# Optimization experiments

Hardware: AMD Instinct MI355X
Metric: run time of the kernel (lower is better)

## Reference

```python
import jax, jax.numpy as jnp
import numpy as np

HID = 16   # hidden_dim
K = 16     # kNN neighbors
B = 64     # graphs per batch
N_TS = 8192
N_LC = 12288


def setup_inputs() -> dict:
    key = jax.random.key(0)
    ks = jax.random.split(key, 24)

    def lin(k, fan_in, fan_out):
        w = jax.random.normal(k, (fan_in, fan_out), jnp.float32) / np.sqrt(fan_in).astype(np.float32)
        return w

    inp = {
        "x_ts": jax.random.normal(ks[0], (N_TS, 6), jnp.float32),
        "x_lc": jax.random.normal(ks[1], (N_LC, 5), jnp.float32),
        # balanced sorted graph ids -> every graph has >= K source nodes
        "batch_ts": jnp.repeat(jnp.arange(B, dtype=jnp.int32), N_TS // B),
        "batch_lc": jnp.repeat(jnp.arange(B, dtype=jnp.int32), N_LC // B),
        # ts_encode: Linear(6,16), ELU, Linear(16,16), ELU
        "ts_w1": lin(ks[2], 6, HID),  "ts_b1": jnp.zeros((HID,), jnp.float32),
        "ts_w2": lin(ks[3], HID, HID), "ts_b2": jnp.zeros((HID,), jnp.float32),
        # lc_encode: Linear(5,16), ELU, Linear(16,16), ELU
        "lc_w1": lin(ks[4], 5, HID),  "lc_b1": jnp.zeros((HID,), jnp.float32),
        "lc_w2": lin(ks[5], HID, HID), "lc_b2": jnp.zeros((HID,), jnp.float32),
        # EdgeConv nn: Linear(2*16, 16), ELU  (shared across the 3 conv calls)
        "conv_w": lin(ks[6], 2 * HID, HID), "conv_b": jnp.zeros((HID,), jnp.float32),
        # output MLP 16->64->32->8->4->1 (ELU between, none after last)
        "out_w1": lin(ks[7], HID, 64), "out_b1": jnp.zeros((64,), jnp.float32),
        "out_w2": lin(ks[8], 64, 32),  "out_b2": jnp.zeros((32,), jnp.float32),
        "out_w3": lin(ks[9], 32, 8),   "out_b3": jnp.zeros((8,), jnp.float32),
        "out_w4": lin(ks[10], 8, 4),   "out_b4": jnp.zeros((4,), jnp.float32),
        "out_w5": lin(ks[11], 4, 1),   "out_b5": jnp.zeros((1,), jnp.float32),
    }
    return inp


def _mlp2(x, w1, b1, w2, b2):
    return jax.nn.elu(jax.nn.elu(x @ w1 + b1) @ w2 + b2)


def _edge_conv(x_src, x_dst, b_src, b_dst, w, b):
    """DynamicEdgeConv: per-graph kNN of dst queries into src, message
    nn(cat[x_i, x_j - x_i]), max-aggregate over the K neighbors."""
    # squared distances [N_dst, N_src]
    d2 = (jnp.sum(x_dst * x_dst, 1)[:, None]
          - 2.0 * (x_dst @ x_src.T)
          + jnp.sum(x_src * x_src, 1)[None, :])
    d2 = jnp.where(b_dst[:, None] == b_src[None, :], d2, jnp.inf)
    _, idx = jax.lax.top_k(-d2, K)          # [N_dst, K] nearest (incl. self when src==dst)
    xj = x_src[idx]                          # [N_dst, K, H] gather
    xi = x_dst[:, None, :]                   # [N_dst, 1, H]
    msg = jnp.concatenate([jnp.broadcast_to(xi, xj.shape), xj - xi], axis=-1)
    msg = jax.nn.elu(msg @ w + b)            # [N_dst, K, H]
    return jnp.max(msg, axis=1)              # max aggregation -> [N_dst, H]


def reference(x_ts, x_lc, batch_ts, batch_lc,
              ts_w1, ts_b1, ts_w2, ts_b2,
              lc_w1, lc_b1, lc_w2, lc_b2,
              conv_w, conv_b,
              out_w1, out_b1, out_w2, out_b2, out_w3, out_b3,
              out_w4, out_b4, out_w5, out_b5):
    x_ts_enc = _mlp2(x_ts, ts_w1, ts_b1, ts_w2, ts_b2)   # [N_ts, 16]
    x_lc_enc = _mlp2(x_lc, lc_w1, lc_b1, lc_w2, lc_b2)   # [N_lc, 16]

    feats1 = _edge_conv(x_lc_enc, x_lc_enc, batch_lc, batch_lc, conv_w, conv_b)  # [N_lc,16]
    feats2 = _edge_conv(x_lc_enc, x_ts_enc, batch_lc, batch_ts, conv_w, conv_b)  # [N_ts,16]
    feats3 = _edge_conv(feats1,   feats2,   batch_lc, batch_ts, conv_w, conv_b)  # [N_ts,16]

    # avg_pool_x(batch_ts, feats3, batch_ts): per-graph mean
    sums = jax.ops.segment_sum(feats3, batch_ts, num_segments=B)
    cnts = jax.ops.segment_sum(jnp.ones((feats3.shape[0],), feats3.dtype), batch_ts, num_segments=B)
    pooled = sums / cnts[:, None]                         # [B, 16]

    h = jax.nn.elu(pooled @ out_w1 + out_b1)
    h = jax.nn.elu(h @ out_w2 + out_b2)
    h = jax.nn.elu(h @ out_w3 + out_b3)
    h = jax.nn.elu(h @ out_w4 + out_b4)
    out = h @ out_w5 + out_b5                             # [B, 1]
    batch_out = jnp.arange(B, dtype=batch_ts.dtype)
    return (out, batch_out)
```

## Files before the change

kernel.cpp:

```cpp
#include <hip/hip_runtime.h>
#include <math.h>

#define HID 16
#define KNN 16
#define NB 64
#define NTS 8192
#define NLC 12288
#define TSG 128
#define LCG 192

__device__ __forceinline__ float eluf(float x) {
    return x > 0.0f ? x : expm1f(x);
}

__device__ __forceinline__ unsigned int f2ord(float f) {
    unsigned int b = __float_as_uint(f);
    return b ^ (((int)b >> 31) | 0x80000000u);
}

__global__ __launch_bounds__(256) void encode_kernel(
    const float* __restrict__ x_ts, const float* __restrict__ x_lc,
    const float* __restrict__ ts_w1, const float* __restrict__ ts_b1,
    const float* __restrict__ ts_w2, const float* __restrict__ ts_b2,
    const float* __restrict__ lc_w1, const float* __restrict__ lc_b1,
    const float* __restrict__ lc_w2, const float* __restrict__ lc_b2,
    const float* __restrict__ cw,
    float* __restrict__ ts_enc, float* __restrict__ lc_enc,
    float* __restrict__ y_lc, float* __restrict__ n_lc,
    float* __restrict__ pooled)
{
    __shared__ float sw1[6 * HID];
    __shared__ float sw2[HID * HID];
    __shared__ float scw2[HID * HID];
    __shared__ float sb1[HID];
    __shared__ float sb2[HID];

    const int tid = threadIdx.x;
    const int t = blockIdx.x * 256 + tid;
    if (t < NB * HID) pooled[t] = 0.0f;

    const bool is_ts = (blockIdx.x < NTS / 256);
    const float* w1 = is_ts ? ts_w1 : lc_w1;
    const float* b1 = is_ts ? ts_b1 : lc_b1;
    const float* w2 = is_ts ? ts_w2 : lc_w2;
    const float* b2 = is_ts ? ts_b2 : lc_b2;
    const int in_dim = is_ts ? 6 : 5;

    if (tid < in_dim * HID) sw1[tid] = w1[tid];
    if (tid < HID * HID)    sw2[tid] = w2[tid];
    if (!is_ts && tid < HID * HID) scw2[tid] = cw[HID * HID + tid];
    if (tid < HID)          { sb1[tid] = b1[tid]; sb2[tid] = b2[tid]; }
    __syncthreads();

    const float* x;
    float* outp;
    int r = 0;
    if (is_ts) { x = x_ts + (size_t)t * 6;          outp = ts_enc + (size_t)t * HID; }
    else       { r = t - NTS; x = x_lc + (size_t)r * 5; outp = lc_enc + (size_t)r * HID; }

    float xin[6];
    for (int k = 0; k < in_dim; ++k) xin[k] = x[k];
    float h[HID];
    #pragma unroll
    for (int c = 0; c < HID; ++c) {
        float s = sb1[c];
        for (int k = 0; k < in_dim; ++k) s += xin[k] * sw1[k * HID + c];
        h[c] = eluf(s);
    }
    float o[HID];
    #pragma unroll
    for (int c = 0; c < HID; ++c) {
        float s = sb2[c];
        #pragma unroll
        for (int k = 0; k < HID; ++k) s += h[k] * sw2[k * HID + c];
        o[c] = eluf(s);
    }
    float4* o4 = reinterpret_cast<float4*>(outp);
    o4[0] = make_float4(o[0],  o[1],  o[2],  o[3]);
    o4[1] = make_float4(o[4],  o[5],  o[6],  o[7]);
    o4[2] = make_float4(o[8],  o[9],  o[10], o[11]);
    o4[3] = make_float4(o[12], o[13], o[14], o[15]);

    if (!is_ts) {
        float nv = 0.f;
        #pragma unroll
        for (int c = 0; c < HID; ++c) nv += o[c] * o[c];
        float y[HID];
        #pragma unroll
        for (int c = 0; c < HID; ++c) {
            float s = 0.f;
            #pragma unroll
            for (int k = 0; k < HID; ++k) s += o[k] * scw2[k * HID + c];
            y[c] = s;
        }
        float4* y4 = reinterpret_cast<float4*>(y_lc + (size_t)r * HID);
        y4[0] = make_float4(y[0],  y[1],  y[2],  y[3]);
        y4[1] = make_float4(y[4],  y[5],  y[6],  y[7]);
        y4[2] = make_float4(y[8],  y[9],  y[10], y[11]);
        y4[3] = make_float4(y[12], y[13], y[14], y[15]);
        n_lc[r] = nv;
    }
}

#define CONV_SMEM_FLOATS (LCG * HID + 2 * HID * HID + 2 * HID)
#define CONV_SMEM_BYTES  (CONV_SMEM_FLOATS * 4)

template<int NSRC, int NDST, bool POOL, bool EPI>
__device__ __forceinline__ void edgeconv_impl(
    float* __restrict__ smem, int bid,
    const float* __restrict__ src, const float* __restrict__ src_y,
    const float* __restrict__ src_n, const float* __restrict__ dst,
    const float* __restrict__ cw, const float* __restrict__ cb,
    float* __restrict__ out_feats, float* __restrict__ out_y,
    float* __restrict__ out_n, float* __restrict__ pool_out)
{
    constexpr int RPB = 8;
    constexpr int BPG = NDST / RPB;
    float* s_y    = smem;
    float* s_dw   = s_y + NSRC * HID;
    float* s_w2   = s_dw + HID * HID;
    float* s_b    = s_w2 + HID * HID;
    float* s_pool = s_b + HID;

    const int tid  = threadIdx.x;
    const int lane = tid & 63;
    const int wave = tid >> 6;
    const int g      = bid / BPG;
    const int rowblk = bid % BPG;

    if (tid < HID * HID) {
        float w1v = cw[tid];
        float w2v = cw[HID * HID + tid];
        s_dw[tid] = w1v - w2v;
        if (EPI) s_w2[tid] = w2v;
    }
    if (tid < HID) s_b[tid] = cb[tid];
    if (POOL && tid < HID) s_pool[tid] = 0.0f;
    {
        const float4* gy = reinterpret_cast<const float4*>(src_y + (size_t)(g * NSRC) * HID);
        float4* sy4 = reinterpret_cast<float4*>(s_y);
        for (int i = tid; i < NSRC * HID / 4; i += 512) sy4[i] = gy[i];
    }

    float rw[3][HID];
    float rn[3];
    #pragma unroll
    for (int k = 0; k < 3; ++k) {
        const float4* rp = reinterpret_cast<const float4*>(src + (size_t)(g * NSRC + lane + 64 * k) * HID);
        float4 a = rp[0], b = rp[1], c4 = rp[2], e = rp[3];
        rw[k][0] = a.x;  rw[k][1] = a.y;  rw[k][2]  = a.z;  rw[k][3]  = a.w;
        rw[k][4] = b.x;  rw[k][5] = b.y;  rw[k][6]  = b.z;  rw[k][7]  = b.w;
        rw[k][8] = c4.x; rw[k][9] = c4.y; rw[k][10] = c4.z; rw[k][11] = c4.w;
        rw[k][12] = e.x; rw[k][13] = e.y; rw[k][14] = e.z;  rw[k][15] = e.w;
        rn[k] = src_n[g * NSRC + lane + 64 * k];
    }

    const int drow = rowblk * RPB + wave;
    const float4* d4 = reinterpret_cast<const float4*>(dst + (size_t)(g * NDST + drow) * HID);
    float xi[HID];
    {
        float4 a = d4[0], b = d4[1], c4 = d4[2], e = d4[3];
        xi[0] = a.x;  xi[1] = a.y;  xi[2]  = a.z;  xi[3]  = a.w;
        xi[4] = b.x;  xi[5] = b.y;  xi[6]  = b.z;  xi[7]  = b.w;
        xi[8] = c4.x; xi[9] = c4.y; xi[10] = c4.z; xi[11] = c4.w;
        xi[12] = e.x; xi[13] = e.y; xi[14] = e.z;  xi[15] = e.w;
    }
    float nd = 0.f;
    #pragma unroll
    for (int c = 0; c < HID; ++c) nd += xi[c] * xi[c];

    unsigned int dk0, dk1, dk2;
    {
        unsigned int dk[3];
        #pragma unroll
        for (int k = 0; k < 3; ++k) {
            float dot = 0.f;
            #pragma unroll
            for (int c = 0; c < HID; ++c) dot += xi[c] * rw[k][c];
            dk[k] = f2ord(nd - 2.0f * dot + rn[k]);
        }
        dk0 = dk[0]; dk1 = dk[1]; dk2 = dk[2];
    }

    unsigned int p = 0;
    int k = KNN;
    for (int b = 31; b >= 0; --b) {
        unsigned int pb = p >> b;
        int cnt = __popcll(__ballot((dk0 >> b) == pb))
                + __popcll(__ballot((dk1 >> b) == pb))
                + __popcll(__ballot((dk2 >> b) == pb));
        if (k > cnt) { k -= cnt; p |= (1u << b); }
    }
    int cnt_eq = __popcll(__ballot(dk0 == p))
               + __popcll(__ballot(dk1 == p))
               + __popcll(__ballot(dk2 == p));
    unsigned int qi = 255u;
    if (cnt_eq != k) {
        qi = 0;
        int kk = k;
        const unsigned int i0 = (unsigned)lane, i1 = (unsigned)(lane + 64), i2 = (unsigned)(lane + 128);
        for (int b = 7; b >= 0; --b) {
            unsigned int qb = qi >> b;
            int cnt = __popcll(__ballot(dk0 == p && (i0 >> b) == qb))
                    + __popcll(__ballot(dk1 == p && (i1 >> b) == qb))
                    + __popcll(__ballot(dk2 == p && (i2 >> b) == qb));
            if (kk > cnt) { kk -= cnt; qi |= (1u << b); }
        }
    }
    unsigned long long m0 = __ballot(dk0 < p || (dk0 == p && (unsigned)lane <= qi));
    unsigned long long m1 = __ballot(dk1 < p || (dk1 == p && (unsigned)(lane + 64) <= qi));
    unsigned long long m2 = __ballot(dk2 < p || (dk2 == p && (unsigned)(lane + 128) <= qi));

    __syncthreads();

    const int c = lane & 15;
    float cic = s_b[c];
    #pragma unroll
    for (int r = 0; r < HID; ++r) cic += xi[r] * s_dw[r * HID + c];

    int jarr[KNN];
    #pragma unroll
    for (int i = 0; i < KNN; ++i) {
        int j;
        if (m0)      { j = __builtin_ctzll(m0);       m0 &= m0 - 1; }
        else if (m1) { j = 64 + __builtin_ctzll(m1);  m1 &= m1 - 1; }
        else         { j = 128 + __builtin_ctzll(m2); m2 &= m2 - 1; }
        jarr[i] = j;
    }
    float yv[KNN];
    #pragma unroll
    for (int i = 0; i < KNN; ++i) yv[i] = s_y[jarr[i] * HID + c];
    float ym = yv[0];
    #pragma unroll
    for (int i = 1; i < KNN; ++i) ym = fmaxf(ym, yv[i]);

    const float f = eluf(cic + ym);

    if (POOL) {
        if (lane < HID) atomicAdd(&s_pool[c], f);
        __syncthreads();
        if (tid < HID) atomicAdd(&pool_out[g * HID + tid], s_pool[tid]);
    } else {
        const int grow = g * NDST + drow;
        if (lane < HID) out_feats[(size_t)grow * HID + c] = f;
        if (EPI) {
            float yvv = 0.f, nv = 0.f;
            #pragma unroll
            for (int r = 0; r < HID; ++r) {
                float fr = __shfl(f, r, 64);
                yvv += fr * s_w2[r * HID + c];
                nv += fr * fr;
            }
            if (lane < HID) out_y[(size_t)grow * HID + c] = yvv;
            if (lane == 0)  out_n[grow] = nv;
        }
    }
}

#define C1_BLOCKS (NB * (LCG / 8))
#define C2_BLOCKS (NB * (TSG / 8))
__global__ __launch_bounds__(512) void edgeconv12_kernel(
    const float* __restrict__ lc_enc, const float* __restrict__ y_lc,
    const float* __restrict__ n_lc, const float* __restrict__ ts_enc,
    const float* __restrict__ cw, const float* __restrict__ cb,
    float* __restrict__ feats1, float* __restrict__ y_f1, float* __restrict__ n_f1,
    float* __restrict__ feats2)
{
    extern __shared__ float smem[];
    if (blockIdx.x < C1_BLOCKS)
        edgeconv_impl<LCG, LCG, false, true>(smem, blockIdx.x, lc_enc, y_lc, n_lc,
                                             lc_enc, cw, cb, feats1, y_f1, n_f1, nullptr);
    else
        edgeconv_impl<LCG, TSG, false, false>(smem, blockIdx.x - C1_BLOCKS, lc_enc, y_lc, n_lc,
                                              ts_enc, cw, cb, feats2, nullptr, nullptr, nullptr);
}

__global__ __launch_bounds__(512) void edgeconv3_kernel(
    const float* __restrict__ feats1, const float* __restrict__ y_f1,
    const float* __restrict__ n_f1, const float* __restrict__ feats2,
    const float* __restrict__ cw, const float* __restrict__ cb,
    float* __restrict__ pooled)
{
    extern __shared__ float smem[];
    edgeconv_impl<LCG, TSG, true, false>(smem, blockIdx.x, feats1, y_f1, n_f1,
                                         feats2, cw, cb, nullptr, nullptr, nullptr, pooled);
}

__global__ __launch_bounds__(64) void head_kernel(
    const float* __restrict__ pooled,
    const float* __restrict__ w1, const float* __restrict__ b1,
    const float* __restrict__ w2, const float* __restrict__ b2,
    const float* __restrict__ w3, const float* __restrict__ b3,
    const float* __restrict__ w4, const float* __restrict__ b4,
    const float* __restrict__ w5, const float* __restrict__ b5,
    float* __restrict__ out)
{
    const int g = blockIdx.x;
    const int lane = threadIdx.x;
    __shared__ float sp[HID];
    __shared__ float sh1[64];
    __shared__ float sh2[32];
    __shared__ float sh3[8];
    __shared__ float sh4[4];

    if (lane < HID) sp[lane] = pooled[g * HID + lane] * (1.0f / (float)TSG);
    __syncthreads();

    {
        float s = b1[lane];
        #pragma unroll
        for (int r = 0; r < HID; ++r) s += sp[r] * w1[r * 64 + lane];
        sh1[lane] = eluf(s);
    }
    __syncthreads();
    if (lane < 32) {
        float s = b2[lane];
        #pragma unroll
        for (int r = 0; r < 64; ++r) s += sh1[r] * w2[r * 32 + lane];
        sh2[lane] = eluf(s);
    }
    __syncthreads();
    if (lane < 8) {
        float s = b3[lane];
        #pragma unroll
        for (int r = 0; r < 32; ++r) s += sh2[r] * w3[r * 8 + lane];
        sh3[lane] = eluf(s);
    }
    __syncthreads();
    if (lane < 4) {
        float s = b4[lane];
        #pragma unroll
        for (int r = 0; r < 8; ++r) s += sh3[r] * w4[r * 4 + lane];
        sh4[lane] = eluf(s);
    }
    __syncthreads();
    if (lane == 0) {
        float s = b5[0];
        #pragma unroll
        for (int r = 0; r < 4; ++r) s += sh4[r] * w5[r];
        out[g] = s;
        out[NB + g] = (float)g;
    }
}

extern "C" void kernel_launch(void* const* d_in, const int* in_sizes, int n_in,
                              void* d_out, int out_size, void* d_ws, size_t ws_size,
                              hipStream_t stream) {
    const float* x_ts  = (const float*)d_in[0];
    const float* x_lc  = (const float*)d_in[1];
    const float* ts_w1 = (const float*)d_in[4];
    const float* ts_b1 = (const float*)d_in[5];
    const float* ts_w2 = (const float*)d_in[6];
    const float* ts_b2 = (const float*)d_in[7];
    const float* lc_w1 = (const float*)d_in[8];
    const float* lc_b1 = (const float*)d_in[9];
    const float* lc_w2 = (const float*)d_in[10];
    const float* lc_b2 = (const float*)d_in[11];
    const float* cw    = (const float*)d_in[12];
    const float* cb    = (const float*)d_in[13];
    const float* ow1   = (const float*)d_in[14];
    const float* ob1   = (const float*)d_in[15];
    const float* ow2   = (const float*)d_in[16];
    const float* ob2   = (const float*)d_in[17];
    const float* ow3   = (const float*)d_in[18];
    const float* ob3   = (const float*)d_in[19];
    const float* ow4   = (const float*)d_in[20];
    const float* ob4   = (const float*)d_in[21];
    const float* ow5   = (const float*)d_in[22];
    const float* ob5   = (const float*)d_in[23];
    float* out = (float*)d_out;

    float* ws = (float*)d_ws;
    float* ts_enc = ws;
    float* lc_enc = ws + 131072;
    float* feats1 = ws + 327680;
    float* feats2 = ws + 524288;
    float* pooled = ws + 655360;
    float* y_lc   = ws + 656384;
    float* n_lc   = ws + 852992;
    float* y_f1   = ws + 865280;
    float* n_f1   = ws + 1061888;

    encode_kernel<<<(NTS + NLC) / 256, 256, 0, stream>>>(
        x_ts, x_lc, ts_w1, ts_b1, ts_w2, ts_b2, lc_w1, lc_b1, lc_w2, lc_b2,
        cw, ts_enc, lc_enc, y_lc, n_lc, pooled);

    edgeconv12_kernel<<<C1_BLOCKS + C2_BLOCKS, 512, CONV_SMEM_BYTES, stream>>>(
        lc_enc, y_lc, n_lc, ts_enc, cw, cb, feats1, y_f1, n_f1, feats2);

    edgeconv3_kernel<<<C2_BLOCKS, 512, CONV_SMEM_BYTES, stream>>>(
        feats1, y_f1, n_f1, feats2, cw, cb, pooled);

    head_kernel<<<NB, 64, 0, stream>>>(
        pooled, ow1, ob1, ow2, ob2, ow3, ob3, ow4, ob4, ow5, ob5, out);
}
```

Baseline: 163.5 us.

## Fuse head MLP into edgeconv3 via last-block counter and split encode rows

The separate head kernel is folded into the third edge-conv kernel. A global atomic counter, reset in the encode kernel, picks the last finishing block, which then runs the output MLP for all 64 graphs, one wave per graph. The encode kernel also now uses 4 threads per row, each computing 4 output channels and sharing hidden activations through shared memory, so it launches four times as many blocks. This removes one kernel launch and raises encode parallelism, at the cost of extra barriers, atomics and a serial tail in a single block.

```diff
diff --git a/kernel.cpp b/kernel.cpp
--- a/kernel.cpp
+++ b/kernel.cpp
@@ -27,19 +27,21 @@
     const float* __restrict__ cw,
     float* __restrict__ ts_enc, float* __restrict__ lc_enc,
     float* __restrict__ y_lc, float* __restrict__ n_lc,
-    float* __restrict__ pooled)
+    float* __restrict__ pooled, int* __restrict__ ctr)
 {
     __shared__ float sw1[6 * HID];
     __shared__ float sw2[HID * HID];
     __shared__ float scw2[HID * HID];
     __shared__ float sb1[HID];
     __shared__ float sb2[HID];
+    __shared__ float s_h[64 * 17];
 
     const int tid = threadIdx.x;
     const int t = blockIdx.x * 256 + tid;
     if (t < NB * HID) pooled[t] = 0.0f;
-
-    const bool is_ts = (blockIdx.x < NTS / 256);
+    if (t == NB * HID) *ctr = 0;
+
+    const bool is_ts = (blockIdx.x < NTS / 64);
     const float* w1 = is_ts ? ts_w1 : lc_w1;
     const float* b1 = is_ts ? ts_b1 : lc_b1;
     const float* w2 = is_ts ? ts_w2 : lc_w2;
@@ -52,53 +54,62 @@
     if (tid < HID)          { sb1[tid] = b1[tid]; sb2[tid] = b2[tid]; }
     __syncthreads();
 
-    const float* x;
-    float* outp;
-    int r = 0;
-    if (is_ts) { x = x_ts + (size_t)t * 6;          outp = ts_enc + (size_t)t * HID; }
-    else       { r = t - NTS; x = x_lc + (size_t)r * 5; outp = lc_enc + (size_t)r * HID; }
+    const int q    = tid & 3;
+    const int rloc = tid >> 2;
+    const int row  = is_ts ? (blockIdx.x * 64 + rloc)
+                           : ((blockIdx.x - 128) * 64 + rloc);
+    const float* x = is_ts ? (x_ts + (size_t)row * 6) : (x_lc + (size_t)row * 5);
+    float* outp    = is_ts ? (ts_enc + (size_t)row * HID) : (lc_enc + (size_t)row * HID);
 
     float xin[6];
     for (int k = 0; k < in_dim; ++k) xin[k] = x[k];
-    float h[HID];
-    #pragma unroll
-    for (int c = 0; c < HID; ++c) {
+
+    #pragma unroll
+    for (int jc = 0; jc < 4; ++jc) {
+        const int c = 4 * q + jc;
         float s = sb1[c];
         for (int k = 0; k < in_dim; ++k) s += xin[k] * sw1[k * HID + c];
-        h[c] = eluf(s);
-    }
-    float o[HID];
-    #pragma unroll
-    for (int c = 0; c < HID; ++c) {
+        s_h[rloc * 17 + c] = eluf(s);
+    }
+    __syncthreads();
+    float hf[HID];
+    #pragma unroll
+    for (int k = 0; k < HID; ++k) hf[k] = s_h[rloc * 17 + k];
+
+    float o4v[4];
+    #pragma unroll
+    for (int jc = 0; jc < 4; ++jc) {
+        const int c = 4 * q + jc;
         float s = sb2[c];
         #pragma unroll
-        for (int k = 0; k < HID; ++k) s += h[k] * sw2[k * HID + c];
-        o[c] = eluf(s);
-    }
-    float4* o4 = reinterpret_cast<float4*>(outp);
-    o4[0] = make_float4(o[0],  o[1],  o[2],  o[3]);
-    o4[1] = make_float4(o[4],  o[5],  o[6],  o[7]);
-    o4[2] = make_float4(o[8],  o[9],  o[10], o[11]);
-    o4[3] = make_float4(o[12], o[13], o[14], o[15]);
+        for (int k = 0; k < HID; ++k) s += hf[k] * sw2[k * HID + c];
+        o4v[jc] = eluf(s);
+    }
+    reinterpret_cast<float4*>(outp)[q] = make_float4(o4v[0], o4v[1], o4v[2], o4v[3]);
 
     if (!is_ts) {
+        __syncthreads();
+        #pragma unroll
+        for (int jc = 0; jc < 4; ++jc) s_h[rloc * 17 + 4 * q + jc] = o4v[jc];
+        __syncthreads();
+        float of[HID];
+        #pragma unroll
+        for (int k = 0; k < HID; ++k) of[k] = s_h[rloc * 17 + k];
         float nv = 0.f;
         #pragma unroll
-        for (int c = 0; c < HID; ++c) nv += o[c] * o[c];
-        float y[HID];
-        #pragma unroll
-        for (int c = 0; c < HID; ++c) {
+        for (int c = 0; c < HID; ++c) nv += of[c] * of[c];
+        float y4[4];
+        #pragma unroll
+        for (int jc = 0; jc < 4; ++jc) {
+            const int c = 4 * q + jc;
             float s = 0.f;
             #pragma unroll
-            for (int k = 0; k < HID; ++k) s += o[k] * scw2[k * HID + c];
-            y[c] = s;
-        }
-        float4* y4 = reinterpret_cast<float4*>(y_lc + (size_t)r * HID);
-        y4[0] = make_float4(y[0],  y[1],  y[2],  y[3]);
-        y4[1] = make_float4(y[4],  y[5],  y[6],  y[7]);
-        y4[2] = make_float4(y[8],  y[9],  y[10], y[11]);
-        y4[3] = make_float4(y[12], y[13], y[14], y[15]);
-        n_lc[r] = nv;
+            for (int k = 0; k < HID; ++k) s += of[k] * scw2[k * HID + c];
+            y4[jc] = s;
+        }
+        reinterpret_cast<float4*>(y_lc + (size_t)row * HID)[q] =
+            make_float4(y4[0], y4[1], y4[2], y4[3]);
+        if (q == 0) n_lc[row] = nv;
     }
 }
 
@@ -279,15 +290,7 @@
     const float* __restrict__ feats1, const float* __restrict__ y_f1,
     const float* __restrict__ n_f1, const float* __restrict__ feats2,
     const float* __restrict__ cw, const float* __restrict__ cb,
-    float* __restrict__ pooled)
-{
-    extern __shared__ float smem[];
-    edgeconv_impl<LCG, TSG, true, false>(smem, blockIdx.x, feats1, y_f1, n_f1,
-                                         feats2, cw, cb, nullptr, nullptr, nullptr, pooled);
-}
-
-__global__ __launch_bounds__(64) void head_kernel(
-    const float* __restrict__ pooled,
+    float* __restrict__ pooled, int* __restrict__ ctr,
     const float* __restrict__ w1, const float* __restrict__ b1,
     const float* __restrict__ w2, const float* __restrict__ b2,
     const float* __restrict__ w3, const float* __restrict__ b3,
@@ -295,51 +298,62 @@
     const float* __restrict__ w5, const float* __restrict__ b5,
     float* __restrict__ out)
 {
-    const int g = blockIdx.x;
-    const int lane = threadIdx.x;
-    __shared__ float sp[HID];
-    __shared__ float sh1[64];
-    __shared__ float sh2[32];
-    __shared__ float sh3[8];
-    __shared__ float sh4[4];
-
-    if (lane < HID) sp[lane] = pooled[g * HID + lane] * (1.0f / (float)TSG);
+    extern __shared__ float smem[];
+    edgeconv_impl<LCG, TSG, true, false>(smem, blockIdx.x, feats1, y_f1, n_f1,
+                                         feats2, cw, cb, nullptr, nullptr, nullptr, pooled);
+
+    __threadfence();
+    __shared__ int s_last;
+    if (threadIdx.x == 0)
+        s_last = (atomicAdd(ctr, 1) == C2_BLOCKS - 1) ? 1 : 0;
     __syncthreads();
-
-    {
-        float s = b1[lane];
-        #pragma unroll
-        for (int r = 0; r < HID; ++r) s += sp[r] * w1[r * 64 + lane];
-        sh1[lane] = eluf(s);
-    }
-    __syncthreads();
-    if (lane < 32) {
-        float s = b2[lane];
-        #pragma unroll
-        for (int r = 0; r < 64; ++r) s += sh1[r] * w2[r * 32 + lane];
-        sh2[lane] = eluf(s);
-    }
-    __syncthreads();
-    if (lane < 8) {
-        float s = b3[lane];
-        #pragma unroll
-        for (int r = 0; r < 32; ++r) s += sh2[r] * w3[r * 8 + lane];
-        sh3[lane] = eluf(s);
-    }
-    __syncthreads();
-    if (lane < 4) {
-        float s = b4[lane];
-        #pragma unroll
-        for (int r = 0; r < 8; ++r) s += sh3[r] * w4[r * 4 + lane];
-        sh4[lane] = eluf(s);
-    }
-    __syncthreads();
-    if (lane == 0) {
-        float s = b5[0];
-        #pragma unroll
-        for (int r = 0; r < 4; ++r) s += sh4[r] * w5[r];
-        out[g] = s;
-        out[NB + g] = (float)g;
+    if (!s_last) return;
+    __threadfence();
+
+    const int lane = threadIdx.x & 63;
+    const int wave = threadIdx.x >> 6;
+    float* hs = smem + wave * 128;
+
+    for (int it = 0; it < 8; ++it) {
+        const int g = it * 8 + wave;
+        if (lane < HID) hs[lane] = pooled[g * HID + lane] * (1.0f / (float)TSG);
+        __syncthreads();
+        {
+            float s = b1[lane];
+            #pragma unroll
+            for (int r = 0; r < HID; ++r) s += hs[r] * w1[r * 64 + lane];
+            hs[16 + lane] = eluf(s);
+        }
+        __syncthreads();
+        if (lane < 32) {
+            float s = b2[lane];
+            #pragma unroll
+            for (int r = 0; r < 64; ++r) s += hs[16 + r] * w2[r * 32 + lane];
+            hs[80 + lane] = eluf(s);
+        }
+        __syncthreads();
+        if (lane < 8) {
+            float s = b3[lane];
+            #pragma unroll
+            for (int r = 0; r < 32; ++r) s += hs[80 + r] * w3[r * 8 + lane];
+            hs[112 + lane] = eluf(s);
+        }
+        __syncthreads();
+        if (lane < 4) {
+            float s = b4[lane];
+            #pragma unroll
+            for (int r = 0; r < 8; ++r) s += hs[112 + r] * w4[r * 4 + lane];
+            hs[120 + lane] = eluf(s);
+        }
+        __syncthreads();
+        if (lane == 0) {
+            float s = b5[0];
+            #pragma unroll
+            for (int r = 0; r < 4; ++r) s += hs[120 + r] * w5[r];
+            out[g] = s;
+            out[NB + g] = (float)g;
+        }
+        __syncthreads();
     }
 }
 
@@ -376,21 +390,20 @@
     float* feats1 = ws + 327680;
     float* feats2 = ws + 524288;
     float* pooled = ws + 655360;
-    float* y_lc   = ws + 656384;
-    float* n_lc   = ws + 852992;
-    float* y_f1   = ws + 865280;
-    float* n_f1   = ws + 1061888;
-
-    encode_kernel<<<(NTS + NLC) / 256, 256, 0, stream>>>(
+    int*   ctr    = (int*)(ws + 656384);
+    float* y_lc   = ws + 656400;
+    float* n_lc   = ws + 853008;
+    float* y_f1   = ws + 865296;
+    float* n_f1   = ws + 1061904;
+
+    encode_kernel<<<(NTS + NLC) / 64, 256, 0, stream>>>(
         x_ts, x_lc, ts_w1, ts_b1, ts_w2, ts_b2, lc_w1, lc_b1, lc_w2, lc_b2,
-        cw, ts_enc, lc_enc, y_lc, n_lc, pooled);
+        cw, ts_enc, lc_enc, y_lc, n_lc, pooled, ctr);
 
     edgeconv12_kernel<<<C1_BLOCKS + C2_BLOCKS, 512, CONV_SMEM_BYTES, stream>>>(
         lc_enc, y_lc, n_lc, ts_enc, cw, cb, feats1, y_f1, n_f1, feats2);
 
     edgeconv3_kernel<<<C2_BLOCKS, 512, CONV_SMEM_BYTES, stream>>>(
-        feats1, y_f1, n_f1, feats2, cw, cb, pooled);
-
-    head_kernel<<<NB, 64, 0, stream>>>(
-        pooled, ow1, ob1, ow2, ob2, ow3, ob3, ow4, ob4, ow5, ob5, out);
-}
+        feats1, y_f1, n_f1, feats2, cw, cb, pooled, ctr,
+        ow1, ob1, ow2, ob2, ow3, ob3, ow4, ob4, ow5, ob5, out);
+}
```

Measured after the change: 314.6 us. 1.92x slower.
